# Performance work log

Hardware: AMD Instinct MI355X
Metric: run time of the kernel (lower is better)

The kernel has to match this reference:

```python
import jax, jax.numpy as jnp
import numpy as np

BLOCK_LEN = 64


def segsum(x):
    """x: (..., T) -> (..., T, T) with segsum[i,j] = sum_{k=j+1..i} x[k] (lower-tri incl diag), -inf above."""
    T = x.shape[-1]
    xc = jnp.cumsum(x, axis=-1)
    seg = xc[..., :, None] - xc[..., None, :]
    mask = jnp.tril(jnp.ones((T, T), dtype=bool))
    return jnp.where(mask, seg, -jnp.inf)


def setup_inputs() -> dict:
    key = jax.random.key(0)
    kx, ka, kb, kc = jax.random.split(key, 4)
    b, s, h, p, n = 4, 4096, 32, 64, 64
    X = jax.random.normal(kx, (b, s, h), dtype=jnp.float32)  # placeholder to keep split order stable
    X = jax.random.normal(kx, (b, s, h, p), dtype=jnp.float32)
    # A must be negative for a stable SSM decay (exp of cumulative sums stays bounded)
    A = -jax.random.uniform(ka, (b, s, h), dtype=jnp.float32, minval=0.0, maxval=1.0)
    B = jax.random.normal(kb, (b, s, h, n), dtype=jnp.float32)
    C = jax.random.normal(kc, (b, s, h, n), dtype=jnp.float32)
    return {"X": X, "A": A, "B": B, "C": C}


def reference(X, A, B, C):
    blk = BLOCK_LEN
    b, s, h, p = X.shape
    n = B.shape[-1]
    c = s // blk
    # chunk: b (c l) ... -> b c l ...
    Xc = X.reshape(b, c, blk, h, p)
    Bc = B.reshape(b, c, blk, h, n)
    Cc = C.reshape(b, c, blk, h, n)
    Ac = A.reshape(b, c, blk, h).transpose(0, 3, 1, 2)  # b h c l
    A_cumsum = jnp.cumsum(Ac, axis=-1)                  # b h c l

    # 1. intra-chunk (diagonal block) output
    L = jnp.exp(segsum(Ac))                             # b h c l s
    Y_diag = jnp.einsum("bclhn,bcshn,bhcls,bcshp->bclhp", Cc, Bc, L, Xc)

    # 2. intra-chunk states (chunk-final state assuming zero initial state)
    decay_states = jnp.exp(A_cumsum[..., -1:] - A_cumsum)
    states = jnp.einsum("bclhn,bhcl,bclhp->bchpn", Bc, decay_states, Xc)

    # 3. inter-chunk recurrence over chunk boundaries
    init = jnp.zeros_like(states[:, :1])
    states = jnp.concatenate([init, states], axis=1)    # b (c+1) h p n
    A_last = jnp.pad(A_cumsum[..., -1], ((0, 0), (0, 0), (1, 0)))  # b h (c+1)
    decay_chunk = jnp.exp(segsum(A_last))               # b h (c+1) (c+1)
    new_states = jnp.einsum("bhzc,bchpn->bzhpn", decay_chunk, states)
    states_in = new_states[:, :-1]                      # state entering each chunk

    # 4. state -> output
    state_decay_out = jnp.exp(A_cumsum)
    Y_off = jnp.einsum("bclhn,bchpn,bhcl->bclhp", Cc, states_in, state_decay_out)

    Y = (Y_diag + Y_off).reshape(b, s, h, p)
    return Y
```

## Files before the change

kernel.cpp:

```cpp
#include <hip/hip_runtime.h>

namespace {

typedef __attribute__((ext_vector_type(8))) short short8;
typedef __attribute__((ext_vector_type(4))) float f32x4;

constexpr int Hh = 32, Ssq = 4096, NCH = 64;
constexpr int GR = 2048;
constexpr int ST = 68;

__device__ inline unsigned short f2bf(float f) {
  unsigned u = __float_as_uint(f);
  u += 0x7FFFu + ((u >> 16) & 1u);
  return (unsigned short)(u >> 16);
}

__device__ inline short8 frag(const unsigned short* p) {
  union { short8 s; uint2 u[2]; } r;
  r.u[0] = *(const uint2*)p;
  r.u[1] = *(const uint2*)(p + 4);
  return r.s;
}

__global__ __launch_bounds__(256)
void k1_states(const float* __restrict__ X0, const float* __restrict__ A0,
               const float* __restrict__ B0, unsigned short* __restrict__ S16) {
  __shared__ unsigned short BTs[64 * ST];
  __shared__ unsigned short XTs[16 * ST];
  __shared__ float ielb[64];
  __shared__ float eab;

  const int tid = threadIdx.x;
  const int pq = blockIdx.x & 3, hi = (blockIdx.x >> 2) & 31, bi = blockIdx.x >> 7;

  const float* Xg = X0 + ((size_t)bi * Ssq * Hh + hi) * 64 + pq * 16;
  const float* Bg = B0 + ((size_t)bi * Ssq * Hh + hi) * 64;
  const float* Ag = A0 + (size_t)bi * Ssq * Hh + hi;
  unsigned short* Sg = S16 + (size_t)(bi * Hh + hi) * NCH * 4096 + pq * 16 * 64;

  const int w = tid >> 6, lane = tid & 63, lr = lane & 15, lk = lane >> 4;
  f32x4 S = {0.f, 0.f, 0.f, 0.f};

  for (int ci = 0; ci < NCH; ++ci) {
    if (tid < 64) {
      float a = Ag[(size_t)(ci * 64 + tid) * Hh];
#pragma unroll
      for (int off = 1; off < 64; off <<= 1) {
        float v = __shfl_up(a, off);
        if (tid >= off) a += v;
      }
      ielb[tid] = __expf(-a);
      if (tid == 63) eab = __expf(a);
    }
    __syncthreads();
    {
      const int r = tid >> 2, cb = (tid & 3) * 4;
      const float iel = ielb[r];
      const float* bp = Bg + (size_t)(ci * 64 + r) * GR;
#pragma unroll
      for (int j = 0; j < 4; ++j) {
        const int c = cb + 16 * j;
        float4 v = *(const float4*)(bp + c);
        BTs[(c + 0) * ST + r] = f2bf(v.x * iel);
        BTs[(c + 1) * ST + r] = f2bf(v.y * iel);
        BTs[(c + 2) * ST + r] = f2bf(v.z * iel);
        BTs[(c + 3) * ST + r] = f2bf(v.w * iel);
      }
      float4 xv = *(const float4*)(Xg + (size_t)(ci * 64 + r) * GR + cb);
      XTs[(cb + 0) * ST + r] = f2bf(xv.x);
      XTs[(cb + 1) * ST + r] = f2bf(xv.y);
      XTs[(cb + 2) * ST + r] = f2bf(xv.z);
      XTs[(cb + 3) * ST + r] = f2bf(xv.w);
    }
    __syncthreads();
    if (ci) {
      unsigned short* sp = Sg + (size_t)ci * 4096;
#pragma unroll
      for (int i = 0; i < 4; ++i)
        sp[(lk * 4 + i) * 64 + w * 16 + lr] = f2bf(S[i]);
    }
    f32x4 acc = S;
#pragma unroll
    for (int ks = 0; ks < 2; ++ks)
      acc = __builtin_amdgcn_mfma_f32_16x16x32_bf16(
          frag(&XTs[lr * ST + ks * 32 + lk * 8]),
          frag(&BTs[(w * 16 + lr) * ST + ks * 32 + lk * 8]), acc, 0, 0, 0);
    const float ea = eab;
#pragma unroll
    for (int i = 0; i < 4; ++i) S[i] = acc[i] * ea;
    __syncthreads();
  }
}

__global__ __launch_bounds__(256, 4)
void k2_y(const float* __restrict__ X0, const float* __restrict__ A0,
          const float* __restrict__ B0, const float* __restrict__ C0,
          const unsigned short* __restrict__ S16, float* __restrict__ Y0) {
  __shared__ unsigned short Cs[64 * ST];
  __shared__ unsigned short Bsh[64 * ST];
  __shared__ unsigned short XT[64 * ST];
  __shared__ unsigned short Sb[64 * ST];
  __shared__ unsigned short Gs[64 * ST];
  __shared__ float elb[64], ielb2[64];

  const int tid = threadIdx.x;
  const int hi = blockIdx.x & 31, ci = (blockIdx.x >> 5) & 63, bi = blockIdx.x >> 11;

  const float* Xg = X0 + (((size_t)bi * Ssq + ci * 64) * Hh + hi) * 64;
  const float* Bg = B0 + (((size_t)bi * Ssq + ci * 64) * Hh + hi) * 64;
  const float* Cg = C0 + (((size_t)bi * Ssq + ci * 64) * Hh + hi) * 64;
  const float* Ag = A0 + ((size_t)bi * Ssq + ci * 64) * Hh + hi;
  const unsigned short* Sg = S16 + ((size_t)(bi * Hh + hi) * NCH + ci) * 4096;
  float* Yg = Y0 + (((size_t)bi * Ssq + ci * 64) * Hh + hi) * 64;

  const int w = tid >> 6, lane = tid & 63, lr = lane & 15, lk = lane >> 4;

  for (int i = tid; i < 64 * ST; i += 256) Gs[i] = 0;

  if (tid < 64) {
    float a = Ag[(size_t)tid * Hh];
#pragma unroll
    for (int off = 1; off < 64; off <<= 1) {
      float v = __shfl_up(a, off);
      if (tid >= off) a += v;
    }
    elb[tid] = __expf(a);
    ielb2[tid] = __expf(-a);
  }
  __syncthreads();

  {
    const int r = tid >> 2, cb = (tid & 3) * 4;
    const float iel = ielb2[r];
    const float* bp = Bg + (size_t)r * GR;
    const float* cp = Cg + (size_t)r * GR;
    const float* xp = Xg + (size_t)r * GR;
#pragma unroll
    for (int j = 0; j < 4; ++j) {
      const int c = cb + 16 * j;
      float4 bv = *(const float4*)(bp + c);
      float4 cv = *(const float4*)(cp + c);
      unsigned short bb[4] = {f2bf(bv.x * iel), f2bf(bv.y * iel),
                              f2bf(bv.z * iel), f2bf(bv.w * iel)};
      unsigned short cc[4] = {f2bf(cv.x), f2bf(cv.y), f2bf(cv.z), f2bf(cv.w)};
      *(uint2*)&Bsh[r * ST + c] = *(const uint2*)bb;
      *(uint2*)&Cs[r * ST + c] = *(const uint2*)cc;
      float4 xv = *(const float4*)(xp + c);
      XT[(c + 0) * ST + r] = f2bf(xv.x);
      XT[(c + 1) * ST + r] = f2bf(xv.y);
      XT[(c + 2) * ST + r] = f2bf(xv.z);
      XT[(c + 3) * ST + r] = f2bf(xv.w);
    }
    if (ci == 0) {
#pragma unroll
      for (int j = 0; j < 4; ++j) {
        const int q = tid + j * 256;
        uint2 z = {0u, 0u};
        *(uint2*)&Sb[(q >> 4) * ST + (q & 15) * 4] = z;
      }
    } else {
#pragma unroll
      for (int j = 0; j < 4; ++j) {
        const int q = tid + j * 256;
        *(uint2*)&Sb[(q >> 4) * ST + (q & 15) * 4] = *(const uint2*)(Sg + q * 4);
      }
    }
  }
  __syncthreads();

  {
    int tl[3] = {-1, -1, -1}, ts[3] = {0, 0, 0};
    switch (w) {
      case 0: tl[0] = 0; ts[0] = 0; tl[1] = 1; ts[1] = 0; tl[2] = 1; ts[2] = 1; break;
      case 1: tl[0] = 2; ts[0] = 0; tl[1] = 2; ts[1] = 1; tl[2] = 2; ts[2] = 2; break;
      case 2: tl[0] = 3; ts[0] = 0; tl[1] = 3; ts[1] = 1; break;
      case 3: tl[0] = 3; ts[0] = 2; tl[1] = 3; ts[1] = 3; break;
    }
#pragma unroll
    for (int t = 0; t < 3; ++t) {
      if (tl[t] >= 0) {
        f32x4 acc = {0.f, 0.f, 0.f, 0.f};
#pragma unroll
        for (int ks = 0; ks < 2; ++ks)
          acc = __builtin_amdgcn_mfma_f32_16x16x32_bf16(
              frag(&Cs[(tl[t] * 16 + lr) * ST + ks * 32 + lk * 8]),
              frag(&Bsh[(ts[t] * 16 + lr) * ST + ks * 32 + lk * 8]), acc, 0, 0, 0);
        const int gcol = ts[t] * 16 + lr;
#pragma unroll
        for (int i = 0; i < 4; ++i) {
          const int grow = tl[t] * 16 + lk * 4 + i;
          float gv = (gcol <= grow) ? acc[i] * elb[grow] : 0.f;
          Gs[grow * ST + gcol] = f2bf(gv);
        }
      }
    }
  }
  __syncthreads();

  {
#pragma unroll
    for (int tp = 0; tp < 4; ++tp) {
      f32x4 aD = {0.f, 0.f, 0.f, 0.f}, aO = {0.f, 0.f, 0.f, 0.f};
#pragma unroll
      for (int ks = 0; ks < 2; ++ks) {
        const int ko = ks * 32 + lk * 8;
        aD = __builtin_amdgcn_mfma_f32_16x16x32_bf16(
            frag(&Gs[(w * 16 + lr) * ST + ko]), frag(&XT[(tp * 16 + lr) * ST + ko]), aD, 0, 0, 0);
        aO = __builtin_amdgcn_mfma_f32_16x16x32_bf16(
            frag(&Cs[(w * 16 + lr) * ST + ko]), frag(&Sb[(tp * 16 + lr) * ST + ko]), aO, 0, 0, 0);
      }
#pragma unroll
      for (int i = 0; i < 4; ++i) {
        const int row = w * 16 + lk * 4 + i;
        Yg[(size_t)row * GR + tp * 16 + lr] = aD[i] + elb[row] * aO[i];
      }
    }
  }
}

}

extern "C" void kernel_launch(void* const* d_in, const int* in_sizes, int n_in,
                              void* d_out, int out_size, void* d_ws, size_t ws_size,
                              hipStream_t stream) {
  const float* X = (const float*)d_in[0];
  const float* A = (const float*)d_in[1];
  const float* B = (const float*)d_in[2];
  const float* C = (const float*)d_in[3];
  float* Y = (float*)d_out;
  unsigned short* S16 = (unsigned short*)d_ws;
  (void)in_sizes; (void)n_in; (void)out_size; (void)ws_size;
  k1_states<<<dim3(512), dim3(256), 0, stream>>>(X, A, B, S16);
  k2_y<<<dim3(8192), dim3(256), 0, stream>>>(X, A, B, C, S16, Y);
}
```

Before: 282.8 us.

## Split sequential state kernel into parallel chunk-state and scan kernels

The old state kernel walked all 64 chunks serially in 512 blocks. It is replaced by two kernels. The first computes each chunk's local final state independently across 8192 blocks. The second runs a light elementwise scan over chunk states using per-chunk decay totals, writing the prefix states in place. This exposes far more parallelism for the state computation, at the cost of an extra launch, extra workspace round-trips and bf16 rounding of the intermediate states before the scan.

```diff
diff --git a/kernel.cpp b/kernel.cpp
--- a/kernel.cpp
+++ b/kernel.cpp
@@ -13,6 +13,9 @@
   unsigned u = __float_as_uint(f);
   u += 0x7FFFu + ((u >> 16) & 1u);
   return (unsigned short)(u >> 16);
+}
+__device__ inline float bf2f(unsigned short s) {
+  return __uint_as_float(((unsigned)s) << 16);
 }
 
 __device__ inline short8 frag(const unsigned short* p) {
@@ -22,73 +25,108 @@
   return r.s;
 }
 
-__global__ __launch_bounds__(256)
-void k1_states(const float* __restrict__ X0, const float* __restrict__ A0,
-               const float* __restrict__ B0, unsigned short* __restrict__ S16) {
+__global__ __launch_bounds__(256, 4)
+void k1a_chunkstate(const float* __restrict__ X0, const float* __restrict__ A0,
+                    const float* __restrict__ B0, unsigned short* __restrict__ S16) {
   __shared__ unsigned short BTs[64 * ST];
-  __shared__ unsigned short XTs[16 * ST];
+  __shared__ unsigned short XTs[64 * ST];
   __shared__ float ielb[64];
   __shared__ float eab;
 
   const int tid = threadIdx.x;
-  const int pq = blockIdx.x & 3, hi = (blockIdx.x >> 2) & 31, bi = blockIdx.x >> 7;
-
-  const float* Xg = X0 + ((size_t)bi * Ssq * Hh + hi) * 64 + pq * 16;
-  const float* Bg = B0 + ((size_t)bi * Ssq * Hh + hi) * 64;
-  const float* Ag = A0 + (size_t)bi * Ssq * Hh + hi;
-  unsigned short* Sg = S16 + (size_t)(bi * Hh + hi) * NCH * 4096 + pq * 16 * 64;
+  const int hi = blockIdx.x & 31, ci = (blockIdx.x >> 5) & 63, bi = blockIdx.x >> 11;
+  if (ci == 63) return;
+
+  const float* Xg = X0 + (((size_t)bi * Ssq + ci * 64) * Hh + hi) * 64;
+  const float* Bg = B0 + (((size_t)bi * Ssq + ci * 64) * Hh + hi) * 64;
+  const float* Ag = A0 + ((size_t)bi * Ssq + ci * 64) * Hh + hi;
+  unsigned short* sp = S16 + ((size_t)(bi * Hh + hi) * NCH + ci) * 4096;
 
   const int w = tid >> 6, lane = tid & 63, lr = lane & 15, lk = lane >> 4;
-  f32x4 S = {0.f, 0.f, 0.f, 0.f};
-
-  for (int ci = 0; ci < NCH; ++ci) {
-    if (tid < 64) {
-      float a = Ag[(size_t)(ci * 64 + tid) * Hh];
-#pragma unroll
-      for (int off = 1; off < 64; off <<= 1) {
-        float v = __shfl_up(a, off);
-        if (tid >= off) a += v;
-      }
-      ielb[tid] = __expf(-a);
-      if (tid == 63) eab = __expf(a);
-    }
-    __syncthreads();
-    {
-      const int r = tid >> 2, cb = (tid & 3) * 4;
-      const float iel = ielb[r];
-      const float* bp = Bg + (size_t)(ci * 64 + r) * GR;
-#pragma unroll
-      for (int j = 0; j < 4; ++j) {
-        const int c = cb + 16 * j;
-        float4 v = *(const float4*)(bp + c);
-        BTs[(c + 0) * ST + r] = f2bf(v.x * iel);
-        BTs[(c + 1) * ST + r] = f2bf(v.y * iel);
-        BTs[(c + 2) * ST + r] = f2bf(v.z * iel);
-        BTs[(c + 3) * ST + r] = f2bf(v.w * iel);
-      }
-      float4 xv = *(const float4*)(Xg + (size_t)(ci * 64 + r) * GR + cb);
-      XTs[(cb + 0) * ST + r] = f2bf(xv.x);
-      XTs[(cb + 1) * ST + r] = f2bf(xv.y);
-      XTs[(cb + 2) * ST + r] = f2bf(xv.z);
-      XTs[(cb + 3) * ST + r] = f2bf(xv.w);
-    }
-    __syncthreads();
-    if (ci) {
-      unsigned short* sp = Sg + (size_t)ci * 4096;
-#pragma unroll
-      for (int i = 0; i < 4; ++i)
-        sp[(lk * 4 + i) * 64 + w * 16 + lr] = f2bf(S[i]);
-    }
-    f32x4 acc = S;
+
+  if (tid < 64) {
+    float a = Ag[(size_t)tid * Hh];
+#pragma unroll
+    for (int off = 1; off < 64; off <<= 1) {
+      float v = __shfl_up(a, off);
+      if (tid >= off) a += v;
+    }
+    ielb[tid] = __expf(-a);
+    if (tid == 63) eab = __expf(a);
+  }
+  __syncthreads();
+
+  {
+    const int r = tid >> 2, cb = (tid & 3) * 4;
+    const float iel = ielb[r];
+    const float* bp = Bg + (size_t)r * GR;
+    const float* xp = Xg + (size_t)r * GR;
+#pragma unroll
+    for (int j = 0; j < 4; ++j) {
+      const int c = cb + 16 * j;
+      float4 bv = *(const float4*)(bp + c);
+      BTs[(c + 0) * ST + r] = f2bf(bv.x * iel);
+      BTs[(c + 1) * ST + r] = f2bf(bv.y * iel);
+      BTs[(c + 2) * ST + r] = f2bf(bv.z * iel);
+      BTs[(c + 3) * ST + r] = f2bf(bv.w * iel);
+      float4 xv = *(const float4*)(xp + c);
+      XTs[(c + 0) * ST + r] = f2bf(xv.x);
+      XTs[(c + 1) * ST + r] = f2bf(xv.y);
+      XTs[(c + 2) * ST + r] = f2bf(xv.z);
+      XTs[(c + 3) * ST + r] = f2bf(xv.w);
+    }
+  }
+  __syncthreads();
+
+  const float ea = eab;
+#pragma unroll
+  for (int tp = 0; tp < 4; ++tp) {
+    f32x4 acc = {0.f, 0.f, 0.f, 0.f};
 #pragma unroll
     for (int ks = 0; ks < 2; ++ks)
       acc = __builtin_amdgcn_mfma_f32_16x16x32_bf16(
-          frag(&XTs[lr * ST + ks * 32 + lk * 8]),
+          frag(&XTs[(tp * 16 + lr) * ST + ks * 32 + lk * 8]),
           frag(&BTs[(w * 16 + lr) * ST + ks * 32 + lk * 8]), acc, 0, 0, 0);
-    const float ea = eab;
-#pragma unroll
-    for (int i = 0; i < 4; ++i) S[i] = acc[i] * ea;
-    __syncthreads();
+#pragma unroll
+    for (int i = 0; i < 4; ++i)
+      sp[(tp * 16 + lk * 4 + i) * 64 + w * 16 + lr] = f2bf(acc[i] * ea);
+  }
+}
+
+__global__ __launch_bounds__(256)
+void k1b_scan(const float* __restrict__ A0, unsigned short* __restrict__ S16) {
+  __shared__ float part[256];
+  __shared__ float eat[64];
+
+  const int tid = threadIdx.x;
+  const int sl8 = blockIdx.x & 7, hi = (blockIdx.x >> 3) & 31, bi = blockIdx.x >> 8;
+  const float* Ag = A0 + (size_t)bi * Ssq * Hh + hi;
+
+  {
+    const int c = tid >> 2, q = tid & 3;
+    float s = 0.f;
+#pragma unroll
+    for (int k = 0; k < 16; ++k) s += Ag[(size_t)(c * 64 + q * 16 + k) * Hh];
+    part[tid] = s;
+  }
+  __syncthreads();
+  if (tid < 64)
+    eat[tid] = __expf(part[tid * 4] + part[tid * 4 + 1] + part[tid * 4 + 2] + part[tid * 4 + 3]);
+  __syncthreads();
+
+  unsigned short* base =
+      S16 + (size_t)(bi * Hh + hi) * NCH * 4096 + sl8 * 512 + tid * 2;
+  float s0 = 0.f, s1 = 0.f;
+  unsigned cur = *(const unsigned*)base;
+  for (int c = 0; c < 63; ++c) {
+    unsigned nxt = 0u;
+    if (c + 1 < 63) nxt = *(const unsigned*)(base + (size_t)(c + 1) * 4096);
+    const float ea = eat[c];
+    s0 = s0 * ea + bf2f((unsigned short)(cur & 0xffffu));
+    s1 = s1 * ea + bf2f((unsigned short)(cur >> 16));
+    *(unsigned*)(base + (size_t)(c + 1) * 4096) =
+        (unsigned)f2bf(s0) | ((unsigned)f2bf(s1) << 16);
+    cur = nxt;
   }
 }
 
@@ -230,6 +268,7 @@
   float* Y = (float*)d_out;
   unsigned short* S16 = (unsigned short*)d_ws;
   (void)in_sizes; (void)n_in; (void)out_size; (void)ws_size;
-  k1_states<<<dim3(512), dim3(256), 0, stream>>>(X, A, B, S16);
+  k1a_chunkstate<<<dim3(8192), dim3(256), 0, stream>>>(X, A, B, S16);
+  k1b_scan<<<dim3(1024), dim3(256), 0, stream>>>(A, S16);
   k2_y<<<dim3(8192), dim3(256), 0, stream>>>(X, A, B, C, S16, Y);
 }
```

New measurement: 244.5 us. -13.6%, faster.
